# Optimization experiments

Measured on AMD Instinct MI355X. Metric: run time of the kernel, lower is better.

The kernel has to match this reference:

```python
import jax, jax.numpy as jnp
import numpy as np

EMB = 1024
HEADS = 16
HEAD_DIM = EMB // HEADS


def setup_inputs() -> dict:
    key = jax.random.key(0)
    ks = jax.random.split(key, 5)
    x = jax.random.normal(ks[0], (4, 2048, EMB), dtype=jnp.float32)
    # qkv Linear: weight [3*EMB, EMB] in torch; store transposed for x @ W
    Wqkv = jax.random.normal(ks[1], (EMB, 3 * EMB), dtype=jnp.float32) * (1.0 / np.sqrt(EMB))
    bqkv = jax.random.normal(ks[2], (3 * EMB,), dtype=jnp.float32) * 0.01
    Wout = jax.random.normal(ks[3], (EMB, EMB), dtype=jnp.float32) * (1.0 / np.sqrt(EMB))
    bout = jax.random.normal(ks[4], (EMB,), dtype=jnp.float32) * 0.01
    return {"x": x, "Wqkv": Wqkv, "bqkv": bqkv, "Wout": Wout, "bout": bout}


def reference(x, Wqkv, bqkv, Wout, bout):
    B, N, _ = x.shape
    qkv = x @ Wqkv + bqkv                              # [B, N, 3*EMB]
    qkv = qkv.reshape(B, N, 3, HEADS, HEAD_DIM)
    q, k, v = jnp.moveaxis(qkv, 2, 0)                  # each [B, N, H, D]
    q = jnp.swapaxes(q, 1, 2)                          # [B, H, N, D]
    k = jnp.swapaxes(k, 1, 2)
    v = jnp.swapaxes(v, 1, 2)
    scale = 1.0 / np.sqrt(HEAD_DIM).astype(np.float32)
    scores = jnp.einsum('bhqd,bhkd->bhqk', q, k) * scale
    attn = jax.nn.softmax(scores, axis=-1)             # dropout p=0 (eval)
    out = jnp.einsum('bhqk,bhkd->bhqd', attn, v)       # [B, H, N, D]
    out = jnp.swapaxes(out, 1, 2).reshape(B, N, EMB)
    return out @ Wout + bout
```

## Files before the change

### kernel.cpp

```cpp
#include <hip/hip_runtime.h>

#define SEQ   2048
#define EMBD  1024
#define HEADS 16
#define HDIM  64
#define MTOT  8192

typedef __attribute__((ext_vector_type(8))) _Float16 half8;
typedef __attribute__((ext_vector_type(4))) _Float16 half4;
typedef __attribute__((ext_vector_type(2))) __fp16 fp16x2;
typedef __attribute__((ext_vector_type(4))) float f32x4;
typedef __attribute__((ext_vector_type(16))) float f32x16;

__device__ __forceinline__ f32x4 mfma16(half8 a, half8 b, f32x4 c) {
  return __builtin_amdgcn_mfma_f32_16x16x32_f16(a, b, c, 0, 0, 0);
}
__device__ __forceinline__ f32x16 mfma32(half8 a, half8 b, f32x16 c) {
  return __builtin_amdgcn_mfma_f32_32x32x16_f16(a, b, c, 0, 0, 0);
}

__device__ __forceinline__ void gload_lds16(const void* g, void* l) {
  __builtin_amdgcn_global_load_lds(
      (const __attribute__((address_space(1))) unsigned int*)g,
      (__attribute__((address_space(3))) unsigned int*)l, 16, 0, 0);
}

__device__ __forceinline__ unsigned pk2(float a, float b) {
  union { fp16x2 v; unsigned u; } t;
  t.v = __builtin_amdgcn_cvt_pkrtz(a, b);
  return t.u;
}

__global__ void k_cvt(const float* __restrict__ in, _Float16* __restrict__ out) {
  size_t i = (size_t)blockIdx.x * blockDim.x + threadIdx.x;
  const f32x4* in4 = (const f32x4*)in;
  f32x4 a = in4[2 * i], b = in4[2 * i + 1];
  half8 h;
  h[0] = (_Float16)a[0]; h[1] = (_Float16)a[1];
  h[2] = (_Float16)a[2]; h[3] = (_Float16)a[3];
  h[4] = (_Float16)b[0]; h[5] = (_Float16)b[1];
  h[6] = (_Float16)b[2]; h[7] = (_Float16)b[3];
  *(half8*)(out + i * 8) = h;
}

__global__ __launch_bounds__(256) void k_transpose(const float* __restrict__ in,
                                                   _Float16* __restrict__ out,
                                                   int R, int C) {
  __shared__ _Float16 tile[64][65];
  const int tid = threadIdx.x;
  const int r0 = blockIdx.y * 64, c0 = blockIdx.x * 64;
  const int tr = tid >> 6;
  const int tc = tid & 63;
  #pragma unroll
  for (int i = 0; i < 16; ++i) {
    const int r = i * 4 + tr;
    tile[r][tc] = (_Float16)in[(size_t)(r0 + r) * C + c0 + tc];
  }
  __syncthreads();
  #pragma unroll
  for (int i = 0; i < 16; ++i) {
    const int cc = i * 4 + tr;
    out[(size_t)(c0 + cc) * R + r0 + tc] = tile[tc][cc];
  }
}

template<int EPI>
__global__ __launch_bounds__(256) void k_gemm(
    const _Float16* __restrict__ A, const _Float16* __restrict__ Bt,
    const float* __restrict__ bias, float* __restrict__ outf,
    _Float16* __restrict__ q, _Float16* __restrict__ k, _Float16* __restrict__ vt)
{
  __shared__ _Float16 sm[2 * 128 * 64];
  _Float16* sA = sm;
  _Float16* sB = sm + 128 * 64;
  const int tid = threadIdx.x;
  const int l = tid & 63, g = l >> 4, c = l & 15;
  const int w = tid >> 6;
  const int wm = (w >> 1) * 64, wn = (w & 1) * 64;
  const int rowBase = blockIdx.y * 128;
  const int colBase = blockIdx.x * 128;

  f32x4 acc[4][4] = {};

  const _Float16* Ag = A + (size_t)(rowBase + (tid >> 3)) * 1024 + (tid & 7) * 8;
  const _Float16* Bg = Bt + (size_t)(colBase + (tid >> 3)) * 1024 + (tid & 7) * 8;
  _Float16* la = sA + tid * 8;
  _Float16* lb = sB + tid * 8;

  for (int kt = 0; kt < 16; ++kt) {
    const _Float16* ag = Ag + kt * 64;
    const _Float16* bg = Bg + kt * 64;
    #pragma unroll
    for (int i = 0; i < 4; ++i) {
      gload_lds16(ag + (size_t)i * 32 * 1024, la + i * 256 * 8);
      gload_lds16(bg + (size_t)i * 32 * 1024, lb + i * 256 * 8);
    }
    __syncthreads();
    #pragma unroll
    for (int kk = 0; kk < 2; ++kk) {
      half8 af[4], bf[4];
      #pragma unroll
      for (int t = 0; t < 4; ++t)
        af[t] = *(const half8*)(sA + (wm + t * 16 + c) * 64 + kk * 32 + g * 8);
      #pragma unroll
      for (int t = 0; t < 4; ++t)
        bf[t] = *(const half8*)(sB + (wn + t * 16 + c) * 64 + kk * 32 + g * 8);
      #pragma unroll
      for (int mt = 0; mt < 4; ++mt)
        #pragma unroll
        for (int nt = 0; nt < 4; ++nt)
          acc[mt][nt] = mfma16(af[mt], bf[nt], acc[mt][nt]);
    }
    __syncthreads();
  }

  #pragma unroll
  for (int mt = 0; mt < 4; ++mt) {
    #pragma unroll
    for (int nt = 0; nt < 4; ++nt) {
      const int col = colBase + wn + nt * 16 + c;
      const float bv = bias[col];
      #pragma unroll
      for (int r = 0; r < 4; ++r) {
        const int row = rowBase + wm + mt * 16 + g * 4 + r;
        const float val = acc[mt][nt][r] + bv;
        if constexpr (EPI == 0) {
          const int s = col >> 10, h = (col >> 6) & 15, d = col & 63;
          const int b = row >> 11, n = row & 2047;
          const int bh = b * HEADS + h;
          const _Float16 hv = (_Float16)val;
          if (s == 2)      vt[((size_t)bh * HDIM + d) * SEQ + n] = hv;
          else if (s == 1) k [((size_t)bh * SEQ + n) * HDIM + d] = hv;
          else             q [((size_t)bh * SEQ + n) * HDIM + d] = hv;
        } else {
          outf[(size_t)row * EMBD + col] = val;
        }
      }
    }
  }
}

__global__ __launch_bounds__(512, 4) void k_attn(
    const _Float16* __restrict__ q, const _Float16* __restrict__ kg,
    const _Float16* __restrict__ vt, _Float16* __restrict__ aout)
{
  __shared__ _Float16 sm[128 * 72 + 64 * 136 + 8 * 32 * 76];
  _Float16* Ks = sm;
  _Float16* Vs = sm + 128 * 72;
  const int tid = threadIdx.x;
  const int w = tid >> 6, l = tid & 63;
  const int q32 = l & 31, hi = l >> 5;
  _Float16* Pw = sm + 128 * 72 + 64 * 136 + w * 32 * 76;

  const int orig = blockIdx.x;
  const int lb = (orig & 7) * 64 + (orig >> 3);
  const int bh = lb >> 3;
  const int n0 = (lb & 7) * 256 + w * 32;

  const _Float16* qb = q  + (size_t)bh * SEQ * HDIM;
  const _Float16* kb = kg + (size_t)bh * SEQ * HDIM;
  const _Float16* vb = vt + (size_t)bh * HDIM * SEQ;
  const int row0 = tid >> 3, cb = tid & 7;

  const _Float16 qs = (_Float16)(0.125f * 1.44269504f);
  half8 aq[4];
  #pragma unroll
  for (int ch = 0; ch < 4; ++ch) {
    half8 t = *(const half8*)(qb + (size_t)(n0 + q32) * HDIM + ch * 16 + hi * 8);
    aq[ch] = t * qs;
  }

  half8 ones;
  #pragma unroll
  for (int i = 0; i < 8; ++i) ones[i] = (_Float16)1.0f;

  float m_ = -1e30f;
  f32x16 o0 = {}, o1 = {}, lacc = {};

  half8 kr0 = *(const half8*)(kb + (size_t)tid * 8);
  half8 kr1 = *(const half8*)(kb + 4096 + (size_t)tid * 8);
  half8 vr0 = *(const half8*)(vb + (size_t)row0 * SEQ + cb * 8);
  half8 vr1 = *(const half8*)(vb + (size_t)row0 * SEQ + 64 + cb * 8);

  for (int kt = 0; kt < SEQ / 128; ++kt) {
    __syncthreads();
    *(half8*)(Ks + row0 * 72 + cb * 8) = kr0;
    *(half8*)(Ks + (row0 + 64) * 72 + cb * 8) = kr1;
    *(half8*)(Vs + row0 * 136 + cb * 8) = vr0;
    *(half8*)(Vs + row0 * 136 + 64 + cb * 8) = vr1;
    if (kt + 1 < SEQ / 128) {
      const _Float16* kn = kb + (size_t)(kt + 1) * 128 * HDIM;
      kr0 = *(const half8*)(kn + (size_t)tid * 8);
      kr1 = *(const half8*)(kn + 4096 + (size_t)tid * 8);
      const _Float16* vn = vb + (size_t)row0 * SEQ + (kt + 1) * 128;
      vr0 = *(const half8*)(vn + cb * 8);
      vr1 = *(const half8*)(vn + 64 + cb * 8);
    }
    __syncthreads();

    #pragma unroll
    for (int p = 0; p < 2; ++p) {
      const _Float16* Kp = Ks + p * 64 * 72;
      const _Float16* Vp = Vs + p * 64;

      f32x16 s0 = {}, s1 = {};
      __builtin_amdgcn_s_setprio(1);
      #pragma unroll
      for (int ch = 0; ch < 4; ++ch) {
        half8 ak0 = *(const half8*)(Kp + q32 * 72 + ch * 16 + hi * 8);
        half8 ak1 = *(const half8*)(Kp + (32 + q32) * 72 + ch * 16 + hi * 8);
        s0 = mfma32(ak0, aq[ch], s0);
        s1 = mfma32(ak1, aq[ch], s1);
      }
      __builtin_amdgcn_s_setprio(0);

      float u0 = fmaxf(s0[0], s1[0]),   u1 = fmaxf(s0[1], s1[1]);
      float u2 = fmaxf(s0[2], s1[2]),   u3 = fmaxf(s0[3], s1[3]);
      float u4 = fmaxf(s0[4], s1[4]),   u5 = fmaxf(s0[5], s1[5]);
      float u6 = fmaxf(s0[6], s1[6]),   u7 = fmaxf(s0[7], s1[7]);
      float u8 = fmaxf(s0[8], s1[8]),   u9 = fmaxf(s0[9], s1[9]);
      float ua = fmaxf(s0[10], s1[10]), ub = fmaxf(s0[11], s1[11]);
      float uc = fmaxf(s0[12], s1[12]), ud = fmaxf(s0[13], s1[13]);
      float ue = fmaxf(s0[14], s1[14]), uf = fmaxf(s0[15], s1[15]);
      u0 = fmaxf(u0, u8); u1 = fmaxf(u1, u9); u2 = fmaxf(u2, ua);
      u3 = fmaxf(u3, ub); u4 = fmaxf(u4, uc); u5 = fmaxf(u5, ud);
      u6 = fmaxf(u6, ue); u7 = fmaxf(u7, uf);
      u0 = fmaxf(u0, u4); u1 = fmaxf(u1, u5); u2 = fmaxf(u2, u6); u3 = fmaxf(u3, u7);
      const float mx = fmaxf(fmaxf(u0, u1), fmaxf(u2, u3));

      if (__any(mx > m_ + 11.5416f)) {
        const float fm = fmaxf(mx, __shfl_xor(mx, 32, 64));
        const float mo = m_;
        const float mn = fmaxf(mo, fm);
        const float cor = __builtin_amdgcn_exp2f(mo - mn);
        m_ = mn;
        lacc[0] *= cor;
        #pragma unroll
        for (int e = 0; e < 16; ++e) { o0[e] *= cor; o1[e] *= cor; }
      }

      #pragma unroll
      for (int e = 0; e < 16; ++e) {
        s0[e] = __builtin_amdgcn_exp2f(s0[e] - m_);
        s1[e] = __builtin_amdgcn_exp2f(s1[e] - m_);
      }

      _Float16* prow = Pw + q32 * 76;
      #pragma unroll
      for (int j = 0; j < 4; ++j) {
        union { unsigned u[2]; half4 h; } t0, t1;
        t0.u[0] = pk2(s0[4 * j], s0[4 * j + 1]);
        t0.u[1] = pk2(s0[4 * j + 2], s0[4 * j + 3]);
        t1.u[0] = pk2(s1[4 * j], s1[4 * j + 1]);
        t1.u[1] = pk2(s1[4 * j + 2], s1[4 * j + 3]);
        *(half4*)(prow + 8 * j + 4 * hi) = t0.h;
        *(half4*)(prow + 32 + 8 * j + 4 * hi) = t1.h;
      }

      __builtin_amdgcn_s_setprio(1);
      #pragma unroll
      for (int ch = 0; ch < 4; ++ch) {
        half8 pf  = *(const half8*)(Pw + q32 * 76 + ch * 16 + hi * 8);
        half8 av0 = *(const half8*)(Vp + q32 * 136 + ch * 16 + hi * 8);
        half8 av1 = *(const half8*)(Vp + (32 + q32) * 136 + ch * 16 + hi * 8);
        o0 = mfma32(av0, pf, o0);
        o1 = mfma32(av1, pf, o1);
        lacc = mfma32(ones, pf, lacc);
      }
      __builtin_amdgcn_s_setprio(0);
    }
  }

  const float rl = __builtin_amdgcn_rcpf(lacc[0]);

  _Float16* Ot = Pw;
  #pragma unroll
  for (int dh = 0; dh < 2; ++dh) {
    #pragma unroll
    for (int j = 0; j < 4; ++j) {
      union { unsigned u[2]; half4 h; } t;
      if (dh == 0) {
        t.u[0] = pk2(o0[4 * j] * rl, o0[4 * j + 1] * rl);
        t.u[1] = pk2(o0[4 * j + 2] * rl, o0[4 * j + 3] * rl);
      } else {
        t.u[0] = pk2(o1[4 * j] * rl, o1[4 * j + 1] * rl);
        t.u[1] = pk2(o1[4 * j + 2] * rl, o1[4 * j + 3] * rl);
      }
      *(half4*)(Ot + q32 * 76 + dh * 32 + 8 * j + 4 * hi) = t.h;
    }
  }

  const int b = bh >> 4, h = bh & 15;
  #pragma unroll
  for (int i = 0; i < 4; ++i) {
    const int qq = 8 * i + (l >> 3);
    half8 v = *(const half8*)(Ot + qq * 76 + (l & 7) * 8);
    *(half8*)(aout + (size_t)(b * SEQ + n0 + qq) * EMBD + h * HDIM + (l & 7) * 8) = v;
  }
}

extern "C" void kernel_launch(void* const* d_in, const int* in_sizes, int n_in,
                              void* d_out, int out_size, void* d_ws, size_t ws_size,
                              hipStream_t stream) {
  const float* x    = (const float*)d_in[0];
  const float* Wqkv = (const float*)d_in[1];
  const float* bqkv = (const float*)d_in[2];
  const float* Wout = (const float*)d_in[3];
  const float* bout = (const float*)d_in[4];
  float* out = (float*)d_out;

  _Float16* ws    = (_Float16*)d_ws;
  _Float16* xh    = ws;
  _Float16* wqkvt = xh + (size_t)MTOT * EMBD;
  _Float16* woutt = wqkvt + (size_t)3 * EMBD * EMBD;
  _Float16* qbuf  = woutt + (size_t)EMBD * EMBD;
  _Float16* kbuf  = qbuf + (size_t)MTOT * EMBD;
  _Float16* vtbuf = kbuf + (size_t)MTOT * EMBD;
  _Float16* aout  = xh;

  k_cvt<<<4096, 256, 0, stream>>>(x, xh);
  k_transpose<<<dim3(48, 16), 256, 0, stream>>>(Wqkv, wqkvt, 1024, 3072);
  k_transpose<<<dim3(16, 16), 256, 0, stream>>>(Wout, woutt, 1024, 1024);
  k_gemm<0><<<dim3(24, 64), 256, 0, stream>>>(xh, wqkvt, bqkv, nullptr,
                                              qbuf, kbuf, vtbuf);
  k_attn<<<512, 512, 0, stream>>>(qbuf, kbuf, vtbuf, aout);
  k_gemm<1><<<dim3(8, 64), 256, 0, stream>>>(aout, woutt, bout, out,
                                             nullptr, nullptr, nullptr);
}
```

Before: 255.2 us.

## Software-pipeline attention tile: compute both QK halves upfront, overlap softmax with PV

Restructures the per-tile attention loop so both 64-key QK^T score blocks are computed with one batch of MFMAs. The second half's max reduction is then interleaved with the first half's PV MFMAs, and the next-tile global prefetch is moved after the first PV. The row-sum is now accumulated with VALU adds plus a final cross-half shuffle instead of an extra MFMA against a ones vector. This removes one MFMA per chunk and is meant to hide softmax latency behind matrix work. In exchange it raises register pressure, holding four score accumulators live, and puts the global loads later in the loop.

```diff
diff --git a/kernel.cpp b/kernel.cpp
--- a/kernel.cpp
+++ b/kernel.cpp
@@ -170,12 +170,8 @@
     aq[ch] = t * qs;
   }
 
-  half8 ones;
-  #pragma unroll
-  for (int i = 0; i < 8; ++i) ones[i] = (_Float16)1.0f;
-
-  float m_ = -1e30f;
-  f32x16 o0 = {}, o1 = {}, lacc = {};
+  float m_ = -1e30f, l_ = 0.f;
+  f32x16 o0 = {}, o1 = {};
 
   half8 kr0 = *(const half8*)(kb + (size_t)tid * 8);
   half8 kr1 = *(const half8*)(kb + 4096 + (size_t)tid * 8);
@@ -188,6 +184,79 @@
     *(half8*)(Ks + (row0 + 64) * 72 + cb * 8) = kr1;
     *(half8*)(Vs + row0 * 136 + cb * 8) = vr0;
     *(half8*)(Vs + row0 * 136 + 64 + cb * 8) = vr1;
+    __syncthreads();
+
+    f32x16 sA0 = {}, sA1 = {}, sB0 = {}, sB1 = {};
+    __builtin_amdgcn_s_setprio(1);
+    #pragma unroll
+    for (int ch = 0; ch < 4; ++ch) {
+      half8 a0 = *(const half8*)(Ks + q32 * 72 + ch * 16 + hi * 8);
+      half8 a1 = *(const half8*)(Ks + (32 + q32) * 72 + ch * 16 + hi * 8);
+      half8 b0 = *(const half8*)(Ks + (64 + q32) * 72 + ch * 16 + hi * 8);
+      half8 b1 = *(const half8*)(Ks + (96 + q32) * 72 + ch * 16 + hi * 8);
+      sA0 = mfma32(a0, aq[ch], sA0);
+      sA1 = mfma32(a1, aq[ch], sA1);
+      sB0 = mfma32(b0, aq[ch], sB0);
+      sB1 = mfma32(b1, aq[ch], sB1);
+    }
+    __builtin_amdgcn_s_setprio(0);
+
+    {
+      float tm[8];
+      #pragma unroll
+      for (int i = 0; i < 8; ++i)
+        tm[i] = fmaxf(fmaxf(sA0[i], sA0[i + 8]), fmaxf(sA1[i], sA1[i + 8]));
+      const float mxA = fmaxf(fmaxf(fmaxf(tm[0], tm[1]), fmaxf(tm[2], tm[3])),
+                              fmaxf(fmaxf(tm[4], tm[5]), fmaxf(tm[6], tm[7])));
+      if (__any(mxA > m_ + 11.5416f)) {
+        const float fm = fmaxf(mxA, __shfl_xor(mxA, 32, 64));
+        const float mn = fmaxf(m_, fm);
+        const float cor = __builtin_amdgcn_exp2f(m_ - mn);
+        m_ = mn; l_ *= cor;
+        #pragma unroll
+        for (int e = 0; e < 16; ++e) { o0[e] *= cor; o1[e] *= cor; }
+      }
+      #pragma unroll
+      for (int e = 0; e < 16; ++e) {
+        sA0[e] = __builtin_amdgcn_exp2f(sA0[e] - m_);
+        sA1[e] = __builtin_amdgcn_exp2f(sA1[e] - m_);
+      }
+      float ts[8];
+      #pragma unroll
+      for (int i = 0; i < 8; ++i)
+        ts[i] = (sA0[i] + sA0[i + 8]) + (sA1[i] + sA1[i + 8]);
+      l_ += ((ts[0] + ts[1]) + (ts[2] + ts[3])) + ((ts[4] + ts[5]) + (ts[6] + ts[7]));
+      _Float16* prow = Pw + q32 * 76;
+      #pragma unroll
+      for (int j = 0; j < 4; ++j) {
+        union { unsigned u[2]; half4 h; } t0, t1;
+        t0.u[0] = pk2(sA0[4 * j], sA0[4 * j + 1]);
+        t0.u[1] = pk2(sA0[4 * j + 2], sA0[4 * j + 3]);
+        t1.u[0] = pk2(sA1[4 * j], sA1[4 * j + 1]);
+        t1.u[1] = pk2(sA1[4 * j + 2], sA1[4 * j + 3]);
+        *(half4*)(prow + 8 * j + 4 * hi) = t0.h;
+        *(half4*)(prow + 32 + 8 * j + 4 * hi) = t1.h;
+      }
+    }
+
+    float tmB[8];
+    #pragma unroll
+    for (int i = 0; i < 8; ++i)
+      tmB[i] = fmaxf(fmaxf(sB0[i], sB0[i + 8]), fmaxf(sB1[i], sB1[i + 8]));
+    const float mxB = fmaxf(fmaxf(fmaxf(tmB[0], tmB[1]), fmaxf(tmB[2], tmB[3])),
+                            fmaxf(fmaxf(tmB[4], tmB[5]), fmaxf(tmB[6], tmB[7])));
+
+    __builtin_amdgcn_s_setprio(1);
+    #pragma unroll
+    for (int ch = 0; ch < 4; ++ch) {
+      half8 pf  = *(const half8*)(Pw + q32 * 76 + ch * 16 + hi * 8);
+      half8 av0 = *(const half8*)(Vs + q32 * 136 + ch * 16 + hi * 8);
+      half8 av1 = *(const half8*)(Vs + (32 + q32) * 136 + ch * 16 + hi * 8);
+      o0 = mfma32(av0, pf, o0);
+      o1 = mfma32(av1, pf, o1);
+    }
+    __builtin_amdgcn_s_setprio(0);
+
     if (kt + 1 < SEQ / 128) {
       const _Float16* kn = kb + (size_t)(kt + 1) * 128 * HDIM;
       kr0 = *(const half8*)(kn + (size_t)tid * 8);
@@ -196,82 +265,53 @@
       vr0 = *(const half8*)(vn + cb * 8);
       vr1 = *(const half8*)(vn + 64 + cb * 8);
     }
-    __syncthreads();
-
-    #pragma unroll
-    for (int p = 0; p < 2; ++p) {
-      const _Float16* Kp = Ks + p * 64 * 72;
-      const _Float16* Vp = Vs + p * 64;
-
-      f32x16 s0 = {}, s1 = {};
-      __builtin_amdgcn_s_setprio(1);
-      #pragma unroll
-      for (int ch = 0; ch < 4; ++ch) {
-        half8 ak0 = *(const half8*)(Kp + q32 * 72 + ch * 16 + hi * 8);
-        half8 ak1 = *(const half8*)(Kp + (32 + q32) * 72 + ch * 16 + hi * 8);
-        s0 = mfma32(ak0, aq[ch], s0);
-        s1 = mfma32(ak1, aq[ch], s1);
-      }
-      __builtin_amdgcn_s_setprio(0);
-
-      float u0 = fmaxf(s0[0], s1[0]),   u1 = fmaxf(s0[1], s1[1]);
-      float u2 = fmaxf(s0[2], s1[2]),   u3 = fmaxf(s0[3], s1[3]);
-      float u4 = fmaxf(s0[4], s1[4]),   u5 = fmaxf(s0[5], s1[5]);
-      float u6 = fmaxf(s0[6], s1[6]),   u7 = fmaxf(s0[7], s1[7]);
-      float u8 = fmaxf(s0[8], s1[8]),   u9 = fmaxf(s0[9], s1[9]);
-      float ua = fmaxf(s0[10], s1[10]), ub = fmaxf(s0[11], s1[11]);
-      float uc = fmaxf(s0[12], s1[12]), ud = fmaxf(s0[13], s1[13]);
-      float ue = fmaxf(s0[14], s1[14]), uf = fmaxf(s0[15], s1[15]);
-      u0 = fmaxf(u0, u8); u1 = fmaxf(u1, u9); u2 = fmaxf(u2, ua);
-      u3 = fmaxf(u3, ub); u4 = fmaxf(u4, uc); u5 = fmaxf(u5, ud);
-      u6 = fmaxf(u6, ue); u7 = fmaxf(u7, uf);
-      u0 = fmaxf(u0, u4); u1 = fmaxf(u1, u5); u2 = fmaxf(u2, u6); u3 = fmaxf(u3, u7);
-      const float mx = fmaxf(fmaxf(u0, u1), fmaxf(u2, u3));
-
-      if (__any(mx > m_ + 11.5416f)) {
-        const float fm = fmaxf(mx, __shfl_xor(mx, 32, 64));
-        const float mo = m_;
-        const float mn = fmaxf(mo, fm);
-        const float cor = __builtin_amdgcn_exp2f(mo - mn);
-        m_ = mn;
-        lacc[0] *= cor;
-        #pragma unroll
-        for (int e = 0; e < 16; ++e) { o0[e] *= cor; o1[e] *= cor; }
-      }
-
-      #pragma unroll
-      for (int e = 0; e < 16; ++e) {
-        s0[e] = __builtin_amdgcn_exp2f(s0[e] - m_);
-        s1[e] = __builtin_amdgcn_exp2f(s1[e] - m_);
-      }
-
+
+    if (__any(mxB > m_ + 11.5416f)) {
+      const float fm = fmaxf(mxB, __shfl_xor(mxB, 32, 64));
+      const float mn = fmaxf(m_, fm);
+      const float cor = __builtin_amdgcn_exp2f(m_ - mn);
+      m_ = mn; l_ *= cor;
+      #pragma unroll
+      for (int e = 0; e < 16; ++e) { o0[e] *= cor; o1[e] *= cor; }
+    }
+    #pragma unroll
+    for (int e = 0; e < 16; ++e) {
+      sB0[e] = __builtin_amdgcn_exp2f(sB0[e] - m_);
+      sB1[e] = __builtin_amdgcn_exp2f(sB1[e] - m_);
+    }
+    {
+      float ts[8];
+      #pragma unroll
+      for (int i = 0; i < 8; ++i)
+        ts[i] = (sB0[i] + sB0[i + 8]) + (sB1[i] + sB1[i + 8]);
+      l_ += ((ts[0] + ts[1]) + (ts[2] + ts[3])) + ((ts[4] + ts[5]) + (ts[6] + ts[7]));
       _Float16* prow = Pw + q32 * 76;
       #pragma unroll
       for (int j = 0; j < 4; ++j) {
         union { unsigned u[2]; half4 h; } t0, t1;
-        t0.u[0] = pk2(s0[4 * j], s0[4 * j + 1]);
-        t0.u[1] = pk2(s0[4 * j + 2], s0[4 * j + 3]);
-        t1.u[0] = pk2(s1[4 * j], s1[4 * j + 1]);
-        t1.u[1] = pk2(s1[4 * j + 2], s1[4 * j + 3]);
+        t0.u[0] = pk2(sB0[4 * j], sB0[4 * j + 1]);
+        t0.u[1] = pk2(sB0[4 * j + 2], sB0[4 * j + 3]);
+        t1.u[0] = pk2(sB1[4 * j], sB1[4 * j + 1]);
+        t1.u[1] = pk2(sB1[4 * j + 2], sB1[4 * j + 3]);
         *(half4*)(prow + 8 * j + 4 * hi) = t0.h;
         *(half4*)(prow + 32 + 8 * j + 4 * hi) = t1.h;
       }
-
-      __builtin_amdgcn_s_setprio(1);
-      #pragma unroll
-      for (int ch = 0; ch < 4; ++ch) {
-        half8 pf  = *(const half8*)(Pw + q32 * 76 + ch * 16 + hi * 8);
-        half8 av0 = *(const half8*)(Vp + q32 * 136 + ch * 16 + hi * 8);
-        half8 av1 = *(const half8*)(Vp + (32 + q32) * 136 + ch * 16 + hi * 8);
-        o0 = mfma32(av0, pf, o0);
-        o1 = mfma32(av1, pf, o1);
-        lacc = mfma32(ones, pf, lacc);
-      }
-      __builtin_amdgcn_s_setprio(0);
-    }
-  }
-
-  const float rl = __builtin_amdgcn_rcpf(lacc[0]);
+    }
+
+    __builtin_amdgcn_s_setprio(1);
+    #pragma unroll
+    for (int ch = 0; ch < 4; ++ch) {
+      half8 pf  = *(const half8*)(Pw + q32 * 76 + ch * 16 + hi * 8);
+      half8 av0 = *(const half8*)(Vs + q32 * 136 + 64 + ch * 16 + hi * 8);
+      half8 av1 = *(const half8*)(Vs + (32 + q32) * 136 + 64 + ch * 16 + hi * 8);
+      o0 = mfma32(av0, pf, o0);
+      o1 = mfma32(av1, pf, o1);
+    }
+    __builtin_amdgcn_s_setprio(0);
+  }
+
+  const float lt = l_ + __shfl_xor(l_, 32, 64);
+  const float rl = __builtin_amdgcn_rcpf(lt);
 
   _Float16* Ot = Pw;
   #pragma unroll
```

After: 404.9 us. +58.6%, slower.
